# Performance work log

Hardware: AMD Instinct MI355X
Metric: run time of the kernel (lower is better)

Reference implementation:

```python
import jax, jax.numpy as jnp
import numpy as np

B, S, HID = 2, 2048, 2048
H, D, KV = 16, 128, 4          # heads, head_dim, kv heads
REP = H // KV                  # GQA repeat factor
THETA = 10000.0


def setup_inputs() -> dict:
    key = jax.random.key(0)
    ks = jax.random.split(key, 12)
    query = jax.random.normal(ks[0], (B, S, HID), jnp.float32)
    k_in = jax.random.normal(ks[1], (B, S, HID), jnp.float32)
    v_in = jax.random.normal(ks[2], (B, S, HID), jnp.float32)
    # additive causal mask: 0 on/below diag, -10000 above
    causal = jnp.tril(jnp.ones((S, S), jnp.float32))
    mask = jnp.broadcast_to((1.0 - causal) * -10000.0, (B, 1, S, S))
    # rotary tables (cos/sin of freqs_cis), shape [S, D//2]
    inv_freq = 1.0 / (THETA ** (jnp.arange(0, D, 2, dtype=jnp.float32) / D))
    ang = jnp.outer(jnp.arange(S, dtype=jnp.float32), inv_freq)
    freqs_cos, freqs_sin = jnp.cos(ang), jnp.sin(ang)
    sd = 0.02
    Wq = jax.random.normal(ks[3], (HID, H * D), jnp.float32) * sd
    bq = jnp.zeros((H * D,), jnp.float32)
    Wk = jax.random.normal(ks[4], (HID, KV * D), jnp.float32) * sd
    bk = jnp.zeros((KV * D,), jnp.float32)
    Wv = jax.random.normal(ks[5], (HID, KV * D), jnp.float32) * sd
    bv = jnp.zeros((KV * D,), jnp.float32)
    Wo = jax.random.normal(ks[6], (H * D, HID), jnp.float32) * sd
    bo = jnp.zeros((HID,), jnp.float32)
    return {"query": query, "key": k_in, "value": v_in, "mask": mask,
            "freqs_cos": freqs_cos, "freqs_sin": freqs_sin,
            "Wq": Wq, "bq": bq, "Wk": Wk, "bk": bk,
            "Wv": Wv, "bv": bv, "Wo": Wo, "bo": bo}


def _rope(x, cos, sin):
    # x: [B,S,h,D]; pairs adjacent dims as complex (view_as_complex)
    xr = x.reshape(*x.shape[:-1], D // 2, 2)
    xe, xo = xr[..., 0], xr[..., 1]
    c = cos[None, :, None, :]
    s = sin[None, :, None, :]
    re = xe * c - xo * s
    im = xe * s + xo * c
    return jnp.stack([re, im], axis=-1).reshape(x.shape)


def reference(query, key, value, mask, freqs_cos, freqs_sin,
              Wq, bq, Wk, bk, Wv, bv, Wo, bo):
    q = (query @ Wq + bq).reshape(B, S, H, D)
    k = (key @ Wk + bk).reshape(B, S, KV, D)
    v = (value @ Wv + bv).reshape(B, S, KV, D)
    # repeat_kv: torch.repeat_interleave along head dim
    k = jnp.repeat(k, REP, axis=2)
    v = jnpp_repeat = jnp.repeat(v, REP, axis=2)
    q = _rope(q, freqs_cos, freqs_sin)
    k = _rope(k, freqs_cos, freqs_sin)
    q = q.transpose(0, 2, 1, 3)  # [B,H,S,D]
    k = k.transpose(0, 2, 1, 3)
    v = v.transpose(0, 2, 1, 3)
    scores = jnp.einsum('bhqd,bhkd->bhqk', q, k) / jnp.sqrt(jnp.float32(D))
    scores = scores + mask
    probs = jax.nn.softmax(scores, axis=-1)
    ctx = jnp.einsum('bhqk,bhkd->bhqd', probs, v)
    ctx = ctx.transpose(0, 2, 1, 3).reshape(B, S, H * D)
    return ctx @ Wo + bo
```

## Files before the change

kernel.cpp:

```cpp
#include <hip/hip_runtime.h>
#include <stdint.h>

#define BB 2
#define SS 2048
#define HID 2048
#define NH 16
#define DD 128
#define NKV 4

typedef unsigned short u16;
typedef __attribute__((ext_vector_type(8))) short short8;
typedef __attribute__((ext_vector_type(4))) float f32x4;

#if __has_builtin(__builtin_amdgcn_exp2f)
#define EXP2(x) __builtin_amdgcn_exp2f(x)
#else
#define EXP2(x) exp2f(x)
#endif

__device__ __forceinline__ u16 f2bf(float x) {
    union { float f; unsigned u; } v; v.f = x;
    unsigned u = v.u;
    return (u16)((u + 0x7FFFu + ((u >> 16) & 1u)) >> 16);
}

__device__ __forceinline__ void async_lds16(const void* g, void* l) {
    __builtin_amdgcn_global_load_lds(
        (const __attribute__((address_space(1))) void*)(uintptr_t)g,
        (__attribute__((address_space(3))) void*)(uintptr_t)l,
        16, 0, 0);
}

__global__ __launch_bounds__(256) void k_prep(const float* __restrict__ query,
                                              const float* __restrict__ key,
                                              const float* __restrict__ value,
                                              const float* __restrict__ Wq,
                                              const float* __restrict__ Wk,
                                              const float* __restrict__ Wv,
                                              const float* __restrict__ Wo,
                                              u16* __restrict__ qbf,
                                              u16* __restrict__ kbf,
                                              u16* __restrict__ vbf,
                                              u16* __restrict__ Wt,
                                              u16* __restrict__ Wot) {
    __shared__ float tile[32][33];
    int x = blockIdx.x;
    if (x < 24576) {
        const float* in; u16* out;
        if (x < 8192)       { in = query; out = qbf; }
        else if (x < 16384) { in = key;   out = kbf; x -= 8192; }
        else                { in = value; out = vbf; x -= 16384; }
        const int i = x * 256 + threadIdx.x;
        float4 v = ((const float4*)in)[i];
        uint2 o;
        o.x = (unsigned)f2bf(v.x) | ((unsigned)f2bf(v.y) << 16);
        o.y = (unsigned)f2bf(v.z) | ((unsigned)f2bf(v.w) << 16);
        ((uint2*)out)[i] = o;
        return;
    }
    const int v_ = x - 24576;
    const int ty = v_ / 160;
    const int xt = v_ - ty * 160;
    const float* src; u16* dst; int N, n0;
    if (xt < 64)      { src = Wq; dst = Wt;                          N = 2048; n0 = xt * 32; }
    else if (xt < 80) { src = Wk; dst = Wt + (size_t)2048 * 2048;    N = 512;  n0 = (xt - 64) * 32; }
    else if (xt < 96) { src = Wv; dst = Wt + (size_t)2560 * 2048;    N = 512;  n0 = (xt - 80) * 32; }
    else              { src = Wo; dst = Wot;                         N = 2048; n0 = (xt - 96) * 32; }
    const int k0 = ty * 32;
    const int c = threadIdx.x & 31, r = threadIdx.x >> 5;
#pragma unroll
    for (int i = 0; i < 32; i += 8)
        tile[r + i][c] = src[(size_t)(k0 + r + i) * N + n0 + c];
    __syncthreads();
#pragma unroll
    for (int i = 0; i < 32; i += 8)
        dst[(size_t)(n0 + r + i) * 2048 + k0 + c] = f2bf(tile[c][r + i]);
}

__device__ __forceinline__ void gemm256_loop(const u16* __restrict__ gA,
                                             const u16* __restrict__ gB,
                                             const int K, char* smem,
                                             const int wave, const int lane,
                                             f32x4 (&acc)[8][4]) {
    const int r = lane & 15, q4 = lane >> 4;
    const int wr = wave >> 2, wc = wave & 3;
    u16* As = (u16*)smem;
    u16* Bs = (u16*)(smem + 65536);

    int aoff[8], boff[4];
#pragma unroll
    for (int i = 0; i < 8; i++) {
        const int ar = wr * 128 + i * 16 + r;
        aoff[i] = ar * 64 + ((q4 ^ (ar & 7)) << 3);
    }
#pragma unroll
    for (int j = 0; j < 4; j++) {
        const int br = wc * 64 + j * 16 + r;
        boff[j] = br * 64 + ((q4 ^ (br & 7)) << 3);
    }

    const int nt = K >> 6;

#define STG_A(buf, i, T) async_lds16(gA + (size_t)(i) * 64 * K + (size_t)(T) * 64, \
                                     smem + (buf) * 32768 + ((i) * 64 + wave * 8) * 128)
#define STG_B(buf, i, T) async_lds16(gB + (size_t)(i) * 64 * K + (size_t)(T) * 64, \
                                     smem + 65536 + (buf) * 32768 + ((i) * 64 + wave * 8) * 128)

    STG_A(0, 0, 0); STG_A(0, 1, 0); STG_A(0, 2, 0); STG_A(0, 3, 0);
    STG_B(0, 0, 0); STG_B(0, 1, 0); STG_B(0, 2, 0); STG_B(0, 3, 0);
    STG_B(1, 0, 1); STG_B(1, 1, 1); STG_B(1, 2, 1); STG_B(1, 3, 1);
    asm volatile("s_waitcnt vmcnt(4)" ::: "memory");
    __builtin_amdgcn_s_barrier();

    short8 Af[4][2], Bf[4][2];
    for (int t = 0; t < nt; t++) {
        const int cur = t & 1;
        const u16* Ab = As + cur * 16384;
        const u16* Bb = Bs + cur * 16384;
        const bool p1v = (t + 1 < nt);
        const bool p2v = (t + 2 < nt);

#pragma unroll
        for (int i = 0; i < 4; i++) {
            Af[i][0] = *(const short8*)(Ab + aoff[i]);
            Af[i][1] = *(const short8*)(Ab + (aoff[i] ^ 32));
        }
#pragma unroll
        for (int j = 0; j < 2; j++) {
            Bf[j][0] = *(const short8*)(Bb + boff[j]);
            Bf[j][1] = *(const short8*)(Bb + (boff[j] ^ 32));
        }
        if (p1v) { STG_A(cur ^ 1, 0, t + 1); STG_A(cur ^ 1, 1, t + 1); }
        __builtin_amdgcn_s_barrier();
        asm volatile("s_waitcnt lgkmcnt(0)" ::: "memory");
        __builtin_amdgcn_s_setprio(1);
#pragma unroll
        for (int kk = 0; kk < 2; kk++)
#pragma unroll
            for (int i = 0; i < 4; i++)
#pragma unroll
                for (int j = 0; j < 2; j++)
                    acc[i][j] = __builtin_amdgcn_mfma_f32_16x16x32_bf16(Af[i][kk], Bf[j][kk], acc[i][j], 0, 0, 0);
        __builtin_amdgcn_s_setprio(0);
        __builtin_amdgcn_s_barrier();

#pragma unroll
        for (int j = 2; j < 4; j++) {
            Bf[j][0] = *(const short8*)(Bb + boff[j]);
            Bf[j][1] = *(const short8*)(Bb + (boff[j] ^ 32));
        }
        if (p1v) { STG_A(cur ^ 1, 2, t + 1); STG_A(cur ^ 1, 3, t + 1); }
        __builtin_amdgcn_s_barrier();
        asm volatile("s_waitcnt lgkmcnt(0)" ::: "memory");
        __builtin_amdgcn_s_setprio(1);
#pragma unroll
        for (int kk = 0; kk < 2; kk++)
#pragma unroll
            for (int i = 0; i < 4; i++)
#pragma unroll
                for (int j = 2; j < 4; j++)
                    acc[i][j] = __builtin_amdgcn_mfma_f32_16x16x32_bf16(Af[i][kk], Bf[j][kk], acc[i][j], 0, 0, 0);
        __builtin_amdgcn_s_setprio(0);
        __builtin_amdgcn_s_barrier();

#pragma unroll
        for (int i = 0; i < 4; i++) {
            Af[i][0] = *(const short8*)(Ab + aoff[i + 4]);
            Af[i][1] = *(const short8*)(Ab + (aoff[i + 4] ^ 32));
        }
        if (p2v) { STG_B(cur, 0, t + 2); STG_B(cur, 1, t + 2); }
        __builtin_amdgcn_s_barrier();
        asm volatile("s_waitcnt lgkmcnt(0)" ::: "memory");
        __builtin_amdgcn_s_setprio(1);
#pragma unroll
        for (int kk = 0; kk < 2; kk++)
#pragma unroll
            for (int i = 0; i < 4; i++)
#pragma unroll
                for (int j = 2; j < 4; j++)
                    acc[i + 4][j] = __builtin_amdgcn_mfma_f32_16x16x32_bf16(Af[i][kk], Bf[j][kk], acc[i + 4][j], 0, 0, 0);
        __builtin_amdgcn_s_setprio(0);
        __builtin_amdgcn_s_barrier();

        if (p2v) {
            STG_B(cur, 2, t + 2); STG_B(cur, 3, t + 2);
            asm volatile("s_waitcnt vmcnt(4)" ::: "memory");
        } else {
            asm volatile("s_waitcnt vmcnt(0)" ::: "memory");
        }
        __builtin_amdgcn_s_barrier();
        __builtin_amdgcn_s_setprio(1);
#pragma unroll
        for (int kk = 0; kk < 2; kk++)
#pragma unroll
            for (int i = 0; i < 4; i++)
#pragma unroll
                for (int j = 0; j < 2; j++)
                    acc[i + 4][j] = __builtin_amdgcn_mfma_f32_16x16x32_bf16(Af[i][kk], Bf[j][kk], acc[i + 4][j], 0, 0, 0);
        __builtin_amdgcn_s_setprio(0);
        __builtin_amdgcn_s_barrier();
    }
#undef STG_A
#undef STG_B
}

__global__ __launch_bounds__(512, 2) void k_gemm_qkv(const u16* __restrict__ qbf,
                                                     const u16* __restrict__ kbf,
                                                     const u16* __restrict__ vbf,
                                                     const u16* __restrict__ Wt,
                                                     const float* __restrict__ bq,
                                                     const float* __restrict__ bk,
                                                     const float* __restrict__ bv,
                                                     const float* __restrict__ fc,
                                                     const float* __restrict__ fs,
                                                     u16* __restrict__ qro,
                                                     u16* __restrict__ kro,
                                                     u16* __restrict__ vtr) {
    __shared__ char smem[131072];
    const int tid = threadIdx.x;
    const int lane = tid & 63, wave = tid >> 6;
    const int wr = wave >> 2, wc = wave & 3;
    const int r = lane & 15, q4 = lane >> 4;
    const int bx = blockIdx.x;
    const int bm0 = blockIdx.y * 256;
    const u16* A = (bx < 8) ? qbf : (bx < 10) ? kbf : vbf;

    const int srow = wave * 8 + (lane >> 3);
    const int c0 = ((lane & 7) ^ (lane >> 3)) * 8;
    const u16* gA = A  + (size_t)(bm0 + srow) * 2048 + c0;
    const u16* gB = Wt + (size_t)(bx * 256 + srow) * 2048 + c0;

    f32x4 acc[8][4] = {};
    gemm256_loop(gA, gB, 2048, smem, wave, lane, acc);

    if (bx < 10) {
        const bool isQ = (bx < 8);
        const float qsc = isQ ? 0.08838834764831845f * 1.4426950408889634f : 1.0f;
        const float* bias = isQ ? bq : bk;
        u16* base = isQ ? qro : kro;
        const int nheads = isQ ? NH : NKV;

        float* ep = (float*)smem + wave * 2560;
#pragma unroll
        for (int j = 0; j < 4; j++) {
            const int gc = bx * 256 + wc * 64 + j * 16;
            const int head = isQ ? (gc >> 7) : ((gc - 2048) >> 7);
            const int d0 = gc & 127;
            const float bcol = bias[head * 128 + d0 + r];
#pragma unroll
            for (int i = 0; i < 8; i++)
#pragma unroll
                for (int g = 0; g < 4; g++)
                    ep[(i * 16 + q4 * 4 + g) * 20 + r] = acc[i][j][g] + bcol;
#pragma unroll
            for (int rr = 0; rr < 2; rr++) {
                const int row = rr * 64 + lane;
                const int grow = bm0 + wr * 128 + row;
                const int s = grow & 2047, bidx = grow >> 11;
                const float* fcp0 = fc + s * 64;
                const float* fsp0 = fs + s * 64;
                float4 x0 = *(float4*)(ep + row * 20 + 0);
                float4 x1 = *(float4*)(ep + row * 20 + 4);
                float4 x2 = *(float4*)(ep + row * 20 + 8);
                float4 x3 = *(float4*)(ep + row * 20 + 12);
                const int ii0 = d0 >> 1;
                float4 ca = *(const float4*)(fcp0 + ii0);
                float4 cb = *(const float4*)(fcp0 + ii0 + 4);
                float4 sa = *(const float4*)(fsp0 + ii0);
                float4 sb = *(const float4*)(fsp0 + ii0 + 4);
                float o[16];
                o[0]  = (x0.x * ca.x - x0.y * sa.x) * qsc;  o[1]  = (x0.x * sa.x + x0.y * ca.x) * qsc;
                o[2]  = (x0.z * ca.y - x0.w * sa.y) * qsc;  o[3]  = (x0.z * sa.y + x0.w * ca.y) * qsc;
                o[4]  = (x1.x * ca.z - x1.y * sa.z) * qsc;  o[5]  = (x1.x * sa.z + x1.y * ca.z) * qsc;
                o[6]  = (x1.z * ca.w - x1.w * sa.w) * qsc;  o[7]  = (x1.z * sa.w + x1.w * ca.w) * qsc;
                o[8]  = (x2.x * cb.x - x2.y * sb.x) * qsc;  o[9]  = (x2.x * sb.x + x2.y * cb.x) * qsc;
                o[10] = (x2.z * cb.y - x2.w * sb.y) * qsc;  o[11] = (x2.z * sb.y + x2.w * cb.y) * qsc;
                o[12] = (x3.x * cb.z - x3.y * sb.z) * qsc;  o[13] = (x3.x * sb.z + x3.y * cb.z) * qsc;
                o[14] = (x3.z * cb.w - x3.w * sb.w) * qsc;  o[15] = (x3.z * sb.w + x3.w * cb.w) * qsc;
                unsigned w0 = (unsigned)f2bf(o[0])  | ((unsigned)f2bf(o[1])  << 16);
                unsigned w1 = (unsigned)f2bf(o[2])  | ((unsigned)f2bf(o[3])  << 16);
                unsigned w2 = (unsigned)f2bf(o[4])  | ((unsigned)f2bf(o[5])  << 16);
                unsigned w3 = (unsigned)f2bf(o[6])  | ((unsigned)f2bf(o[7])  << 16);
                unsigned w4 = (unsigned)f2bf(o[8])  | ((unsigned)f2bf(o[9])  << 16);
                unsigned w5 = (unsigned)f2bf(o[10]) | ((unsigned)f2bf(o[11]) << 16);
                unsigned w6 = (unsigned)f2bf(o[12]) | ((unsigned)f2bf(o[13]) << 16);
                unsigned w7 = (unsigned)f2bf(o[14]) | ((unsigned)f2bf(o[15]) << 16);
                u16* dst = base + (((size_t)(bidx * nheads + head) * SS + s) << 7) + d0;
                *(uint4*)dst = make_uint4(w0, w1, w2, w3);
                *(uint4*)(dst + 8) = make_uint4(w4, w5, w6, w7);
            }
        }
    } else {
#pragma unroll
        for (int j = 0; j < 4; j++) {
            const int colb = bx * 256 + wc * 64 + j * 16 + r - 2560;
            const int d = colb & 127, kv = colb >> 7;
            const float bb = bv[colb];
#pragma unroll
            for (int i = 0; i < 8; i++) {
                const int row0 = bm0 + wr * 128 + i * 16 + q4 * 4;
                const int s0 = row0 & 2047, b = row0 >> 11;
                uint2 o;
                o.x = (unsigned)f2bf(acc[i][j][0] + bb) | ((unsigned)f2bf(acc[i][j][1] + bb) << 16);
                o.y = (unsigned)f2bf(acc[i][j][2] + bb) | ((unsigned)f2bf(acc[i][j][3] + bb) << 16);
                *(uint2*)(vtr + ((size_t)(b * NKV + kv) * DD + d) * SS + s0) = o;
            }
        }
    }
}

__global__ __launch_bounds__(512, 2) void k_gemm_bt(const u16* __restrict__ A,
                                                    const u16* __restrict__ Bt,
                                                    const float* __restrict__ bias,
                                                    float* __restrict__ C,
                                                    int M, int N, int K) {
    __shared__ char smem[131072];
    const int tid = threadIdx.x;
    const int lane = tid & 63, wave = tid >> 6;
    const int wr = wave >> 2, wc = wave & 3;
    const int r = lane & 15, q4 = lane >> 4;
    const int bm0 = blockIdx.y * 256, bn0 = blockIdx.x * 256;

    const int srow = wave * 8 + (lane >> 3);
    const int c0 = ((lane & 7) ^ (lane >> 3)) * 8;
    const u16* gA = A  + (size_t)(bm0 + srow) * K + c0;
    const u16* gB = Bt + (size_t)(bn0 + srow) * K + c0;

    f32x4 acc[8][4] = {};
    gemm256_loop(gA, gB, K, smem, wave, lane, acc);

#pragma unroll
    for (int j = 0; j < 4; j++) {
        const int col = bn0 + wc * 64 + j * 16 + r;
        const float bb = bias[col];
#pragma unroll
        for (int i = 0; i < 8; i++) {
            const int row = bm0 + wr * 128 + i * 16 + q4 * 4;
#pragma unroll
            for (int g = 0; g < 4; g++)
                C[(size_t)(row + g) * N + col] = acc[i][j][g] + bb;
        }
    }
}

__global__ __launch_bounds__(256) void k_attn(const u16* __restrict__ Q,
                                              const u16* __restrict__ K_,
                                              const u16* __restrict__ V_,
                                              u16* __restrict__ Ctx) {
    __shared__ u16 Ks[32 * 128];
    __shared__ u16 Vs[128 * 32];
    __shared__ u16 Pb[4 * 32 * 40];

    const int tid = threadIdx.x;
    const int lane = tid & 63, wave = tid >> 6;
    const int bh = blockIdx.x;
    const int b = bh >> 4, h = bh & 15;
    const int kvh = (b << 2) | (h >> 2);
    const int qb = (gridDim.y - 1 - blockIdx.y) * 128;
    const int qcol = lane & 15, q4 = lane >> 4;
    const int qw = qb + wave * 32;

    const u16* Qg = Q + ((size_t)bh * SS + qw + qcol) * DD;
    short8 qfr[2][4];
#pragma unroll
    for (int qi = 0; qi < 2; qi++)
#pragma unroll
        for (int c = 0; c < 4; c++)
            qfr[qi][c] = *(const short8*)(Qg + qi * 16 * DD + c * 32 + q4 * 8);

    const u16* Kg = K_ + (size_t)kvh * SS * DD;
    const u16* Vg = V_ + (size_t)kvh * DD * SS;

    const int krow = tid >> 4;
    const int kchunk = (tid & 15) ^ (krow & 7);
    const int vd = tid >> 2;
    const int vchunk = (tid & 3) ^ ((vd >> 1) & 3);

    f32x4 lacc[2] = {};
    f32x4 oacc[2][8] = {};

    const short8 ones = {0x3F80, 0x3F80, 0x3F80, 0x3F80, 0x3F80, 0x3F80, 0x3F80, 0x3F80};
    u16* pb = Pb + wave * 1280;
    unsigned* pb32 = (unsigned*)pb;

    for (int kb = 0; kb < qb + 128; kb += 32) {
        async_lds16(Kg + (size_t)(kb + krow) * DD + kchunk * 8,       Ks + wave * 512);
        async_lds16(Kg + (size_t)(kb + 16 + krow) * DD + kchunk * 8,  Ks + 2048 + wave * 512);
        async_lds16(Vg + (size_t)vd * SS + kb + vchunk * 8,           Vs + wave * 512);
        async_lds16(Vg + (size_t)(vd + 64) * SS + kb + vchunk * 8,    Vs + 2048 + wave * 512);
        __syncthreads();

        if (kb <= qw + 31) {
            f32x4 sc[2][2] = {};
#pragma unroll
            for (int kt = 0; kt < 2; kt++) {
                const int kr = kt * 16 + qcol;
#pragma unroll
                for (int c = 0; c < 4; c++) {
                    short8 kf = *(const short8*)(Ks + kr * 128 + (((c * 4 + q4) ^ (kr & 7)) << 3));
                    sc[kt][0] = __builtin_amdgcn_mfma_f32_16x16x32_bf16(kf, qfr[0][c], sc[kt][0], 0, 0, 0);
                    sc[kt][1] = __builtin_amdgcn_mfma_f32_16x16x32_bf16(kf, qfr[1][c], sc[kt][1], 0, 0, 0);
                }
            }

            if (kb + 32 > qw) {
#pragma unroll
                for (int kt = 0; kt < 2; kt++)
#pragma unroll
                    for (int qi = 0; qi < 2; qi++)
#pragma unroll
                        for (int g = 0; g < 4; g++) {
                            const int key = kb + kt * 16 + q4 * 4 + g;
                            if (key > qw + qi * 16 + qcol) sc[kt][qi][g] = -1e30f;
                        }
            }

            const unsigned sel = 0x07060302u;
#pragma unroll
            for (int qi = 0; qi < 2; qi++) {
                float p0 = EXP2(sc[0][qi][0]), p1 = EXP2(sc[0][qi][1]);
                float p2 = EXP2(sc[0][qi][2]), p3 = EXP2(sc[0][qi][3]);
                float p4 = EXP2(sc[1][qi][0]), p5 = EXP2(sc[1][qi][1]);
                float p6 = EXP2(sc[1][qi][2]), p7 = EXP2(sc[1][qi][3]);
                unsigned pk0 = __builtin_amdgcn_perm(__float_as_uint(p1), __float_as_uint(p0), sel);
                unsigned pk1 = __builtin_amdgcn_perm(__float_as_uint(p3), __float_as_uint(p2), sel);
                unsigned pk2 = __builtin_amdgcn_perm(__float_as_uint(p5), __float_as_uint(p4), sel);
                unsigned pk3 = __builtin_amdgcn_perm(__float_as_uint(p7), __float_as_uint(p6), sel);
                const int row = qi * 16 + qcol;
                *(uint2*)(pb32 + row * 20 + 2 * q4)     = make_uint2(pk0, pk1);
                *(uint2*)(pb32 + row * 20 + 8 + 2 * q4) = make_uint2(pk2, pk3);
            }

            short8 pf0 = *(const short8*)(pb + qcol * 40 + q4 * 8);
            short8 pf1 = *(const short8*)(pb + (16 + qcol) * 40 + q4 * 8);

            lacc[0] = __builtin_amdgcn_mfma_f32_16x16x32_bf16(ones, pf0, lacc[0], 0, 0, 0);
            lacc[1] = __builtin_amdgcn_mfma_f32_16x16x32_bf16(ones, pf1, lacc[1], 0, 0, 0);
#pragma unroll
            for (int dt = 0; dt < 8; dt++) {
                const int vr = dt * 16 + qcol;
                short8 vfr = *(const short8*)(Vs + vr * 32 + ((q4 ^ ((vr >> 1) & 3)) << 3));
                oacc[0][dt] = __builtin_amdgcn_mfma_f32_16x16x32_bf16(vfr, pf0, oacc[0][dt], 0, 0, 0);
                oacc[1][dt] = __builtin_amdgcn_mfma_f32_16x16x32_bf16(vfr, pf1, oacc[1][dt], 0, 0, 0);
            }
        }
        __syncthreads();
    }

#pragma unroll
    for (int qi = 0; qi < 2; qi++) {
        const float inv = 1.0f / lacc[qi][0];
        u16* outp = Ctx + ((size_t)b * SS + qw + qi * 16 + qcol) * (NH * DD) + h * DD;
#pragma unroll
        for (int dt = 0; dt < 8; dt++) {
            unsigned lo = (unsigned)f2bf(oacc[qi][dt][0] * inv) | ((unsigned)f2bf(oacc[qi][dt][1] * inv) << 16);
            unsigned hi = (unsigned)f2bf(oacc[qi][dt][2] * inv) | ((unsigned)f2bf(oacc[qi][dt][3] * inv) << 16);
            *(uint2*)(outp + dt * 16 + q4 * 4) = make_uint2(lo, hi);
        }
    }
}

extern "C" void kernel_launch(void* const* d_in, const int* in_sizes, int n_in,
                              void* d_out, int out_size, void* d_ws, size_t ws_size,
                              hipStream_t stream) {
    const float* query = (const float*)d_in[0];
    const float* key   = (const float*)d_in[1];
    const float* value = (const float*)d_in[2];
    const float* fc    = (const float*)d_in[4];
    const float* fs    = (const float*)d_in[5];
    const float* Wq    = (const float*)d_in[6];
    const float* bq    = (const float*)d_in[7];
    const float* Wk    = (const float*)d_in[8];
    const float* bk    = (const float*)d_in[9];
    const float* Wv    = (const float*)d_in[10];
    const float* bv    = (const float*)d_in[11];
    const float* Wo    = (const float*)d_in[12];
    const float* bo    = (const float*)d_in[13];
    float* out = (float*)d_out;

    char* w = (char*)d_ws;
    u16* qbf = (u16*)(w);
    u16* kbf = (u16*)(w + 16777216);
    u16* vbf = (u16*)(w + 33554432);
    u16* Wt  = (u16*)(w + 50331648);
    u16* Wot = (u16*)(w + 62914560);
    u16* qro = (u16*)(w + 71303168);
    u16* kro = (u16*)(w + 88080384);
    u16* vtr = (u16*)(w + 92274688);
    u16* ctx = (u16*)(w + 96468992);

    k_prep<<<34816, 256, 0, stream>>>(query, key, value, Wq, Wk, Wv, Wo,
                                      qbf, kbf, vbf, Wt, Wot);
    k_gemm_qkv<<<dim3(12, 16), 512, 0, stream>>>(qbf, kbf, vbf, Wt, bq, bk, bv,
                                                 fc, fs, qro, kro, vtr);
    k_attn<<<dim3(32, 16), 256, 0, stream>>>(qro, kro, vtr, ctx);
    k_gemm_bt<<<dim3(8, 16), 512, 0, stream>>>(ctx, Wot, bo, out, 4096, 2048, 2048);
}
```

Baseline: 405.4 us.

## Triple-buffer attention K/V loads and swizzle GEMM block order

The attention kernel now prefetches K/V tiles two iterations ahead into a three-slot LDS ring, waiting with a partial vmcnt plus barrier instead of a full syncthreads, so loads overlap compute. It raises wave priority around the MFMA sections and pads the P buffer stride from 40 to 48. Both GEMM kernels remap block indices so consecutive blocks share A rows or B columns, for better L2 reuse. The tripled LDS use may lower attention occupancy, and the overrun stages are clamped to the last tile, which issues redundant loads.

```diff
diff --git a/kernel.cpp b/kernel.cpp
--- a/kernel.cpp
+++ b/kernel.cpp
@@ -221,8 +221,12 @@
     const int lane = tid & 63, wave = tid >> 6;
     const int wr = wave >> 2, wc = wave & 3;
     const int r = lane & 15, q4 = lane >> 4;
-    const int bx = blockIdx.x;
-    const int bm0 = blockIdx.y * 256;
+
+    const int bid0 = blockIdx.y * 12 + blockIdx.x;
+    const int nb = (bid0 & 7) * 24 + (bid0 >> 3);
+    const int bx = nb % 12;
+    const int bm0 = (nb / 12) * 256;
+
     const u16* A = (bx < 8) ? qbf : (bx < 10) ? kbf : vbf;
 
     const int srow = wave * 8 + (lane >> 3);
@@ -319,7 +323,11 @@
     const int lane = tid & 63, wave = tid >> 6;
     const int wr = wave >> 2, wc = wave & 3;
     const int r = lane & 15, q4 = lane >> 4;
-    const int bm0 = blockIdx.y * 256, bn0 = blockIdx.x * 256;
+
+    const int bid0 = blockIdx.y * 8 + blockIdx.x;
+    const int nb = (bid0 & 7) * 16 + (bid0 >> 3);
+    const int bn0 = (nb % 8) * 256;
+    const int bm0 = (nb / 8) * 256;
 
     const int srow = wave * 8 + (lane >> 3);
     const int c0 = ((lane & 7) ^ (lane >> 3)) * 8;
@@ -347,9 +355,9 @@
                                               const u16* __restrict__ K_,
                                               const u16* __restrict__ V_,
                                               u16* __restrict__ Ctx) {
-    __shared__ u16 Ks[32 * 128];
-    __shared__ u16 Vs[128 * 32];
-    __shared__ u16 Pb[4 * 32 * 40];
+    __shared__ u16 Ks[3][32 * 128];
+    __shared__ u16 Vs[3][128 * 32];
+    __shared__ u16 Pb[4][32 * 48];
 
     const int tid = threadIdx.x;
     const int lane = tid & 63, wave = tid >> 6;
@@ -376,32 +384,49 @@
     const int vd = tid >> 2;
     const int vchunk = (tid & 3) ^ ((vd >> 1) & 3);
 
+    const int nt = (qb + 128) >> 5;
+    const int kmax = (nt - 1) * 32;
+
     f32x4 lacc[2] = {};
     f32x4 oacc[2][8] = {};
 
     const short8 ones = {0x3F80, 0x3F80, 0x3F80, 0x3F80, 0x3F80, 0x3F80, 0x3F80, 0x3F80};
-    u16* pb = Pb + wave * 1280;
+    u16* pb = &Pb[wave][0];
     unsigned* pb32 = (unsigned*)pb;
 
-    for (int kb = 0; kb < qb + 128; kb += 32) {
-        async_lds16(Kg + (size_t)(kb + krow) * DD + kchunk * 8,       Ks + wave * 512);
-        async_lds16(Kg + (size_t)(kb + 16 + krow) * DD + kchunk * 8,  Ks + 2048 + wave * 512);
-        async_lds16(Vg + (size_t)vd * SS + kb + vchunk * 8,           Vs + wave * 512);
-        async_lds16(Vg + (size_t)(vd + 64) * SS + kb + vchunk * 8,    Vs + 2048 + wave * 512);
-        __syncthreads();
+#define STAGE_KV(T, BUF) do {                                                            \
+        const int kb_ = min((T) * 32, kmax);                                             \
+        async_lds16(Kg + (size_t)(kb_ + krow) * DD + kchunk * 8,      &Ks[BUF][0] + wave * 512); \
+        async_lds16(Kg + (size_t)(kb_ + 16 + krow) * DD + kchunk * 8, &Ks[BUF][0] + 2048 + wave * 512); \
+        async_lds16(Vg + (size_t)vd * SS + kb_ + vchunk * 8,          &Vs[BUF][0] + wave * 512); \
+        async_lds16(Vg + (size_t)(vd + 64) * SS + kb_ + vchunk * 8,   &Vs[BUF][0] + 2048 + wave * 512); \
+    } while (0)
+
+    STAGE_KV(0, 0);
+    STAGE_KV(1, 1);
+    asm volatile("s_waitcnt vmcnt(4)\n\ts_barrier" ::: "memory");
+
+    for (int t = 0; t < nt; t++) {
+        const int kb = t * 32;
+        const int cur = t % 3;
+        STAGE_KV(t + 2, (t + 2) % 3);
+        const u16* Ksc = &Ks[cur][0];
+        const u16* Vsc = &Vs[cur][0];
 
         if (kb <= qw + 31) {
             f32x4 sc[2][2] = {};
+            __builtin_amdgcn_s_setprio(1);
 #pragma unroll
             for (int kt = 0; kt < 2; kt++) {
                 const int kr = kt * 16 + qcol;
 #pragma unroll
                 for (int c = 0; c < 4; c++) {
-                    short8 kf = *(const short8*)(Ks + kr * 128 + (((c * 4 + q4) ^ (kr & 7)) << 3));
+                    short8 kf = *(const short8*)(Ksc + kr * 128 + (((c * 4 + q4) ^ (kr & 7)) << 3));
                     sc[kt][0] = __builtin_amdgcn_mfma_f32_16x16x32_bf16(kf, qfr[0][c], sc[kt][0], 0, 0, 0);
                     sc[kt][1] = __builtin_amdgcn_mfma_f32_16x16x32_bf16(kf, qfr[1][c], sc[kt][1], 0, 0, 0);
                 }
             }
+            __builtin_amdgcn_s_setprio(0);
 
             if (kb + 32 > qw) {
 #pragma unroll
@@ -427,25 +452,28 @@
                 unsigned pk2 = __builtin_amdgcn_perm(__float_as_uint(p5), __float_as_uint(p4), sel);
                 unsigned pk3 = __builtin_amdgcn_perm(__float_as_uint(p7), __float_as_uint(p6), sel);
                 const int row = qi * 16 + qcol;
-                *(uint2*)(pb32 + row * 20 + 2 * q4)     = make_uint2(pk0, pk1);
-                *(uint2*)(pb32 + row * 20 + 8 + 2 * q4) = make_uint2(pk2, pk3);
+                *(uint2*)(pb32 + row * 24 + 2 * q4)     = make_uint2(pk0, pk1);
+                *(uint2*)(pb32 + row * 24 + 8 + 2 * q4) = make_uint2(pk2, pk3);
             }
 
-            short8 pf0 = *(const short8*)(pb + qcol * 40 + q4 * 8);
-            short8 pf1 = *(const short8*)(pb + (16 + qcol) * 40 + q4 * 8);
-
+            short8 pf0 = *(const short8*)(pb + qcol * 48 + q4 * 8);
+            short8 pf1 = *(const short8*)(pb + (16 + qcol) * 48 + q4 * 8);
+
+            __builtin_amdgcn_s_setprio(1);
             lacc[0] = __builtin_amdgcn_mfma_f32_16x16x32_bf16(ones, pf0, lacc[0], 0, 0, 0);
             lacc[1] = __builtin_amdgcn_mfma_f32_16x16x32_bf16(ones, pf1, lacc[1], 0, 0, 0);
 #pragma unroll
             for (int dt = 0; dt < 8; dt++) {
                 const int vr = dt * 16 + qcol;
-                short8 vfr = *(const short8*)(Vs + vr * 32 + ((q4 ^ ((vr >> 1) & 3)) << 3));
+                short8 vfr = *(const short8*)(Vsc + vr * 32 + ((q4 ^ ((vr >> 1) & 3)) << 3));
                 oacc[0][dt] = __builtin_amdgcn_mfma_f32_16x16x32_bf16(vfr, pf0, oacc[0][dt], 0, 0, 0);
                 oacc[1][dt] = __builtin_amdgcn_mfma_f32_16x16x32_bf16(vfr, pf1, oacc[1][dt], 0, 0, 0);
             }
-        }
-        __syncthreads();
-    }
+            __builtin_amdgcn_s_setprio(0);
+        }
+        asm volatile("s_waitcnt vmcnt(4)\n\ts_barrier" ::: "memory");
+    }
+#undef STAGE_KV
 
 #pragma unroll
     for (int qi = 0; qi < 2; qi++) {
```

Result: no change. 404.3 us (-0.3%).
